# Kernel tuning notes

Measured on AMD Instinct MI355X. Metric: run time of the kernel, lower is better.

The kernel has to match this reference:

```python
import jax, jax.numpy as jnp
import numpy as np

B, N, D, H = 2, 2048, 1024, 16
DH = D // H  # head dim = 64


def setup_inputs() -> dict:
    key = jax.random.key(0)
    k1, k2, k3 = jax.random.split(key, 3)
    x = jax.random.normal(k1, (B, N, D), dtype=jnp.float32)
    # per-head Linear(D, 3*DH): stacked weights (H, D, 3*DH), biases (H, 3*DH)
    W_qkv = jax.random.normal(k2, (H, D, 3 * DH), dtype=jnp.float32) * 0.02
    b_qkv = jnp.zeros((H, 3 * DH), dtype=jnp.float32)
    W_proj = jax.random.normal(k3, (D, D), dtype=jnp.float32) * 0.02
    b_proj = jnp.zeros((D,), dtype=jnp.float32)
    return {"x": x, "W_qkv": W_qkv, "b_qkv": b_qkv, "W_proj": W_proj, "b_proj": b_proj}


def reference(x, W_qkv, b_qkv, W_proj, b_proj):
    b, n, d = x.shape
    h = W_qkv.shape[0]
    dh = W_qkv.shape[2] // 3
    # all heads' kqv projections at once: (B, H, N, 3*DH)
    qkv = jnp.einsum('bnd,hde->bhne', x, W_qkv) + b_qkv[None, :, None, :]
    # original chunks in order k, q, v
    k, q, v = jnp.split(qkv, 3, axis=-1)  # each (B, H, N, DH)
    # scores[b,h,n,m] = q_n . k_m / sqrt(dh)
    scores = jnp.einsum('bhnd,bhmd->bhnm', q, k) / jnp.sqrt(jnp.asarray(dh, x.dtype))
    causal = jnp.tril(jnp.ones((n, n), dtype=bool))
    scores = jnp.where(causal[None, None, :, :], scores, -jnp.inf)
    A = jax.nn.softmax(scores, axis=-1)
    out = jnp.einsum('bhnm,bhmd->bhnd', A, v)
    # concat heads (head-major order matches the torch cat over head list)
    out = out.transpose(0, 2, 1, 3).reshape(b, n, h * dh)
    return out @ W_proj + b_proj
```

## Files before the change

### kernel.cpp

```cpp
#include <hip/hip_runtime.h>
#include <hip/hip_bf16.h>

typedef __hip_bfloat16 HBF;
typedef __bf16 bf16x8 __attribute__((ext_vector_type(8)));
typedef __bf16 bf16x4 __attribute__((ext_vector_type(4)));
typedef float f32x4 __attribute__((ext_vector_type(4)));
typedef float float4v __attribute__((ext_vector_type(4)));

__device__ __forceinline__ float toF(float x) { return x; }
__device__ __forceinline__ float toF(HBF x) { return __bfloat162float(x); }

#define MFMA16(a, b, c) __builtin_amdgcn_mfma_f32_16x16x32_bf16((a), (b), (c), 0, 0, 0)
#define EXP2F(x) __builtin_amdgcn_exp2f(x)
#define QSCALE 0.18033688011112042f
#define MEMFENCE asm volatile("" ::: "memory")

__device__ __forceinline__ void gload_lds16(const HBF* g, HBF* l) {
  __builtin_amdgcn_global_load_lds((const __attribute__((address_space(1))) void*)g,
                                   (__attribute__((address_space(3))) void*)l, 16, 0, 0);
}

__global__ void prep_k(const float* __restrict__ x, HBF* __restrict__ xb,
                       const float* __restrict__ Wqkv, HBF* __restrict__ wqkv_t,
                       const float* __restrict__ Wproj, HBF* __restrict__ wproj_t) {
  const int bid = blockIdx.x, tid = threadIdx.x;
  if (bid < 4096) {
    int i = bid * 256 + tid;
    float4v a = reinterpret_cast<const float4v*>(x)[i];
    HBF o[4] = {__float2bfloat16(a.x), __float2bfloat16(a.y),
                __float2bfloat16(a.z), __float2bfloat16(a.w)};
    *reinterpret_cast<ulonglong1*>(&xb[i * 4]) = *reinterpret_cast<ulonglong1*>(o);
    return;
  }
  __shared__ float tile[32][33];
  const float* in;
  HBF* out;
  int R, C, gx, gy;
  size_t base;
  if (bid < 7168) {
    int t = bid - 4096;
    int gz = t / 192, rem = t % 192;
    gy = rem / 6; gx = rem % 6;
    R = 1024; C = 192;
    base = (size_t)gz * R * C;
    in = Wqkv; out = wqkv_t;
  } else {
    int t = bid - 7168;
    gy = t / 32; gx = t % 32;
    R = 1024; C = 1024;
    base = 0;
    in = Wproj; out = wproj_t;
  }
  int r0 = gy * 32, c0 = gx * 32;
  int tx = tid & 31, ty = tid >> 5;
#pragma unroll
  for (int i = ty; i < 32; i += 8)
    tile[i][tx] = in[base + (size_t)(r0 + i) * C + c0 + tx];
  __syncthreads();
#pragma unroll
  for (int i = ty; i < 32; i += 8)
    out[base + (size_t)(c0 + i) * R + r0 + tx] = __float2bfloat16(tile[tx][i]);
}

__launch_bounds__(512, 4)
__global__ void gemm_qkv_8ph(const HBF* __restrict__ A, const HBF* __restrict__ Bt,
                             const float* __restrict__ bias,
                             HBF* __restrict__ Kout, HBF* __restrict__ Qout,
                             HBF* __restrict__ Vtout) {
  __shared__ __align__(16) HBF As[2][8192];
  __shared__ __align__(16) HBF Bs[2][12288];
  const int tid = threadIdx.x, lane = tid & 63, w = tid >> 6;
  const int lo = lane & 15, g4 = lane >> 4;
  const int wr = w >> 2, wc = w & 3;
  const int s = ((int)blockIdx.x & 7) * 64 + ((int)blockIdx.x >> 3);
  const int bx = s & 15, by = s >> 4;
  const int m0 = by * 128, n0 = bx * 192;
  const int NT = 16;

  f32x4 acc[4][3];
#pragma unroll
  for (int i = 0; i < 4; i++)
#pragma unroll
    for (int j = 0; j < 3; j++) acc[i][j] = (f32x4){0.f, 0.f, 0.f, 0.f};
  bf16x8 af[4][2], bfr[3][2];

  const int rl0 = w * 8 + (lane >> 3);
  const int rl1 = 64 + rl0;
  const int kc0 = (lane & 7) ^ (rl0 & 7);
  const int kc1 = (lane & 7) ^ (rl1 & 7);

  auto stageA = [&](int kt) {
    HBF* base = &As[kt & 1][0];
    gload_lds16(A + (size_t)(m0 + rl0) * 1024 + kt * 64 + kc0 * 8, base + w * 512);
    gload_lds16(A + (size_t)(m0 + rl1) * 1024 + kt * 64 + kc1 * 8, base + 4096 + w * 512);
  };
  auto stageB = [&](int kt, int g) {
    gload_lds16(Bt + (size_t)(n0 + g * 64 + rl0) * 1024 + kt * 64 + kc0 * 8,
                &Bs[kt & 1][g * 4096] + w * 512);
  };
  auto ldA = [&](int bb, int mt, int ks) -> bf16x8 {
    int row = wr * 64 + mt * 16 + lo;
    return *reinterpret_cast<const bf16x8*>(&As[bb][row * 64 + ((ks * 32 + g4 * 8) ^ ((row & 7) * 8))]);
  };
  auto ldB = [&](int bb, int nt, int ks) -> bf16x8 {
    int row = wc * 48 + nt * 16 + lo;
    return *reinterpret_cast<const bf16x8*>(&Bs[bb][row * 64 + ((ks * 32 + g4 * 8) ^ ((row & 7) * 8))]);
  };

  stageA(0); stageB(0, 0); stageB(0, 1); stageB(0, 2);
  stageA(1);
  asm volatile("s_waitcnt vmcnt(2)" ::: "memory");
  __builtin_amdgcn_s_barrier();
  MEMFENCE;

  for (int t = 0; t < NT; ++t) {
    const int bb = t & 1;
#pragma unroll
    for (int mt = 0; mt < 4; ++mt) { af[mt][0] = ldA(bb, mt, 0); af[mt][1] = ldA(bb, mt, 1); }
#pragma unroll
    for (int nt = 0; nt < 2; ++nt) { bfr[nt][0] = ldB(bb, nt, 0); bfr[nt][1] = ldB(bb, nt, 1); }
    if (t + 1 < NT) stageB(t + 1, 0);
    MEMFENCE; __builtin_amdgcn_s_barrier(); MEMFENCE;
    __builtin_amdgcn_s_setprio(1);
#pragma unroll
    for (int mt = 0; mt < 4; ++mt)
#pragma unroll
      for (int nt = 0; nt < 2; ++nt)
#pragma unroll
        for (int ks = 0; ks < 2; ++ks) acc[mt][nt] = MFMA16(af[mt][ks], bfr[nt][ks], acc[mt][nt]);
    __builtin_amdgcn_s_setprio(0);
    MEMFENCE; __builtin_amdgcn_s_barrier(); MEMFENCE;
    bfr[2][0] = ldB(bb, 2, 0); bfr[2][1] = ldB(bb, 2, 1);
    if (t + 1 < NT) { stageB(t + 1, 1); stageB(t + 1, 2); }
    if (t + 2 < NT) stageA(t + 2);
    MEMFENCE; __builtin_amdgcn_s_barrier(); MEMFENCE;
    __builtin_amdgcn_s_setprio(1);
#pragma unroll
    for (int mt = 0; mt < 4; ++mt)
#pragma unroll
      for (int ks = 0; ks < 2; ++ks) acc[mt][2] = MFMA16(af[mt][ks], bfr[2][ks], acc[mt][2]);
    __builtin_amdgcn_s_setprio(0);
    if (t + 2 < NT) {
      asm volatile("s_waitcnt vmcnt(2)" ::: "memory");
    } else {
      asm volatile("s_waitcnt vmcnt(0)" ::: "memory");
    }
    __builtin_amdgcn_s_barrier();
    MEMFENCE;
  }

#pragma unroll
  for (int mt = 0; mt < 4; ++mt) {
    int mrow = m0 + wr * 64 + mt * 16 + g4 * 4;
#pragma unroll
    for (int nt = 0; nt < 3; ++nt) {
      int e = wc * 48 + nt * 16 + lo;
      float bv = bias[bx * 192 + e];
#pragma unroll
      for (int r = 0; r < 4; ++r) {
        int mm = mrow + r;
        int b = mm >> 11, n = mm & 2047;
        float v = acc[mt][nt][r] + bv;
        size_t bh64 = (size_t)(b * 16 + bx);
        if (e < 64)       Kout[(bh64 * 2048 + n) * 64 + e] = __float2bfloat16(v);
        else if (e < 128) Qout[(bh64 * 2048 + n) * 64 + e - 64] = __float2bfloat16(v * QSCALE);
        else              Vtout[(bh64 * 64 + (e - 128)) * 2048 + n] = __float2bfloat16(v);
      }
    }
  }
}

__launch_bounds__(256, 3)
__global__ void gemm_proj_k(const HBF* __restrict__ A, const HBF* __restrict__ Bt,
                            const float* __restrict__ bias, float* __restrict__ Cout) {
  __shared__ __align__(16) HBF As[2][4096];
  __shared__ __align__(16) HBF Bs[2][8192];
  const int tid = threadIdx.x, lane = tid & 63, w = tid >> 6;
  const int lo = lane & 15, g4 = lane >> 4;
  const int wrp = w >> 1, wcp = w & 1;
  const int s = ((int)blockIdx.x & 7) * 64 + ((int)blockIdx.x >> 3);
  const int bxn = s & 7, by = s >> 3;
  const int m0 = by * 64, n0 = bxn * 128;
  const int NT = 16;

  f32x4 acc[2][4];
#pragma unroll
  for (int i = 0; i < 2; i++)
#pragma unroll
    for (int j = 0; j < 4; j++) acc[i][j] = (f32x4){0.f, 0.f, 0.f, 0.f};
  bf16x8 af[2][2], bfr[4][2];

  const int rr = tid >> 3;
  const int ch = tid & 7;

  auto stageA = [&](int kt, int h) {
    int row = h * 32 + rr;
    gload_lds16(A + (size_t)(m0 + row) * 1024 + kt * 64 + ((ch ^ (row & 7)) * 8),
                &As[kt & 1][h * 2048] + w * 512);
  };
  auto stageB = [&](int kt, int g) {
    int row = g * 32 + rr;
    gload_lds16(Bt + (size_t)(n0 + row) * 1024 + kt * 64 + ((ch ^ (row & 7)) * 8),
                &Bs[kt & 1][g * 2048] + w * 512);
  };
  auto ldA = [&](int bb, int mt, int ks) -> bf16x8 {
    int row = wrp * 32 + mt * 16 + lo;
    return *reinterpret_cast<const bf16x8*>(&As[bb][row * 64 + ((ks * 32 + g4 * 8) ^ ((row & 7) * 8))]);
  };
  auto ldB = [&](int bb, int nt, int ks) -> bf16x8 {
    int row = wcp * 64 + nt * 16 + lo;
    return *reinterpret_cast<const bf16x8*>(&Bs[bb][row * 64 + ((ks * 32 + g4 * 8) ^ ((row & 7) * 8))]);
  };

  stageA(0, 0); stageA(0, 1);
  stageB(0, 0); stageB(0, 1); stageB(0, 2); stageB(0, 3);
  stageA(1, 0); stageA(1, 1);
  asm volatile("s_waitcnt vmcnt(2)" ::: "memory");
  __builtin_amdgcn_s_barrier();
  MEMFENCE;

  for (int t = 0; t < NT; ++t) {
    const int bb = t & 1;
#pragma unroll
    for (int mt = 0; mt < 2; ++mt) { af[mt][0] = ldA(bb, mt, 0); af[mt][1] = ldA(bb, mt, 1); }
#pragma unroll
    for (int nt = 0; nt < 2; ++nt) { bfr[nt][0] = ldB(bb, nt, 0); bfr[nt][1] = ldB(bb, nt, 1); }
    if (t + 1 < NT) { stageB(t + 1, 0); stageB(t + 1, 1); }
    MEMFENCE; __builtin_amdgcn_s_barrier(); MEMFENCE;
    __builtin_amdgcn_s_setprio(1);
#pragma unroll
    for (int mt = 0; mt < 2; ++mt)
#pragma unroll
      for (int nt = 0; nt < 2; ++nt)
#pragma unroll
        for (int ks = 0; ks < 2; ++ks) acc[mt][nt] = MFMA16(af[mt][ks], bfr[nt][ks], acc[mt][nt]);
    __builtin_amdgcn_s_setprio(0);
    MEMFENCE; __builtin_amdgcn_s_barrier(); MEMFENCE;
#pragma unroll
    for (int nt = 2; nt < 4; ++nt) { bfr[nt][0] = ldB(bb, nt, 0); bfr[nt][1] = ldB(bb, nt, 1); }
    if (t + 1 < NT) { stageB(t + 1, 2); stageB(t + 1, 3); }
    if (t + 2 < NT) { stageA(t + 2, 0); stageA(t + 2, 1); }
    MEMFENCE; __builtin_amdgcn_s_barrier(); MEMFENCE;
    __builtin_amdgcn_s_setprio(1);
#pragma unroll
    for (int mt = 0; mt < 2; ++mt)
#pragma unroll
      for (int nt = 2; nt < 4; ++nt)
#pragma unroll
        for (int ks = 0; ks < 2; ++ks) acc[mt][nt] = MFMA16(af[mt][ks], bfr[nt][ks], acc[mt][nt]);
    __builtin_amdgcn_s_setprio(0);
    if (t + 2 < NT) {
      asm volatile("s_waitcnt vmcnt(2)" ::: "memory");
    } else {
      asm volatile("s_waitcnt vmcnt(0)" ::: "memory");
    }
    __builtin_amdgcn_s_barrier();
    MEMFENCE;
  }

#pragma unroll
  for (int mt = 0; mt < 2; ++mt) {
    int mrow = m0 + wrp * 32 + mt * 16 + g4 * 4;
#pragma unroll
    for (int nt = 0; nt < 4; ++nt) {
      int col = n0 + wcp * 64 + nt * 16 + lo;
      float bv = bias[col];
#pragma unroll
      for (int r = 0; r < 4; ++r)
        Cout[(size_t)(mrow + r) * 1024 + col] = acc[mt][nt][r] + bv;
    }
  }
}

__launch_bounds__(256, 4)
__global__ void attn_fwd_k(const HBF* __restrict__ Qb, const HBF* __restrict__ Kb,
                           const HBF* __restrict__ Vt, HBF* __restrict__ Ob) {
  __shared__ __align__(16) HBF Ks[2][4096];
  __shared__ __align__(16) HBF Vs[2][4096];
  __shared__ __align__(16) HBF pLds[4][2048];
  const int tid = threadIdx.x;
  const int lane = tid & 63;
  const int w = tid >> 6;
  const int lo = lane & 15, g4 = lane >> 4;

  const int lin = blockIdx.x;
  const int xcd = lin & 7, c = lin >> 3;
  const int bh = xcd * 4 + (c & 3);
  const int j = 31 - (c >> 2);
  const int b = bh >> 4, h = bh & 15;
  const int qrow0 = j * 64 + w * 16;
  const int nkv = (j + 2) >> 1;

  const HBF* Qp = Qb + (size_t)bh * 2048 * 64;
  const HBF* Kp = Kb + (size_t)bh * 2048 * 64;
  const HBF* Vp = Vt + (size_t)bh * 64 * 2048;

  bf16x8 qf[2];
#pragma unroll
  for (int ds = 0; ds < 2; ds++)
    qf[ds] = *reinterpret_cast<const bf16x8*>(Qp + (size_t)(qrow0 + lo) * 64 + ds * 32 + g4 * 8);

  const f32x4 zero = {0.f, 0.f, 0.f, 0.f};
  f32x4 o[4];
  float m = -1e30f, l = 0.f;
#pragma unroll
  for (int j4 = 0; j4 < 4; j4++) o[j4] = zero;

  const int srow = (lane >> 3) & 7;
  const int sch = lane & 7;
  const int psw = (lo & 7) << 4;

  auto stage = [&](int kv0) {
#pragma unroll
    for (int sub = 0; sub < 2; sub++)
#pragma unroll
      for (int cc = 0; cc < 2; cc++) {
        int seg = w * 2 + cc;
        int row = seg * 8 + srow;
        gload_lds16(Kp + (size_t)(kv0 + sub * 64 + row) * 64 + ((sch ^ (row & 7)) * 8),
                    &Ks[sub][seg * 512]);
        gload_lds16(Vp + (size_t)row * 2048 + kv0 + sub * 64 + ((sch ^ (row & 7)) * 8),
                    &Vs[sub][seg * 512]);
      }
  };

  for (int t = 0; t < nkv; ++t) {
    const int kv0 = t * 128;
    stage(kv0);
    __syncthreads();

    f32x4 st[2][4];
#pragma unroll
    for (int sub = 0; sub < 2; sub++)
#pragma unroll
      for (int kt = 0; kt < 4; kt++) {
        int krow = kt * 16 + lo;
        bf16x8 kf0 = *reinterpret_cast<const bf16x8*>(&Ks[sub][krow * 64 + ((g4 ^ (krow & 7)) * 8)]);
        bf16x8 kf1 = *reinterpret_cast<const bf16x8*>(&Ks[sub][krow * 64 + (((4 + g4) ^ (krow & 7)) * 8)]);
        f32x4 z = zero;
        z = MFMA16(kf0, qf[0], z);
        z = MFMA16(kf1, qf[1], z);
        st[sub][kt] = z;
      }

    const int q = qrow0 + lo;
    float pmax = -1e30f;
    if (t == nkv - 1) {
#pragma unroll
      for (int sub = 0; sub < 2; sub++)
#pragma unroll
        for (int kt = 0; kt < 4; kt++)
#pragma unroll
          for (int r = 0; r < 4; r++) {
            int key = kv0 + sub * 64 + kt * 16 + g4 * 4 + r;
            float v = (key <= q) ? st[sub][kt][r] : -1e30f;
            st[sub][kt][r] = v;
            pmax = fmaxf(pmax, v);
          }
    } else {
#pragma unroll
      for (int sub = 0; sub < 2; sub++)
#pragma unroll
        for (int kt = 0; kt < 4; kt++)
#pragma unroll
          for (int r = 0; r < 4; r++) pmax = fmaxf(pmax, st[sub][kt][r]);
    }
    pmax = fmaxf(pmax, __shfl_xor(pmax, 16));
    pmax = fmaxf(pmax, __shfl_xor(pmax, 32));
    if (__any(pmax > m + 11.5f)) {
      float mn = fmaxf(m, pmax);
      float al = EXP2F(m - mn);
      m = mn;
      l *= al;
      float alr[4];
#pragma unroll
      for (int r = 0; r < 4; r++) alr[r] = __shfl(al, g4 * 4 + r);
#pragma unroll
      for (int j4 = 0; j4 < 4; j4++)
#pragma unroll
        for (int r = 0; r < 4; r++) o[j4][r] *= alr[r];
    }
#pragma unroll
    for (int sub = 0; sub < 2; sub++)
#pragma unroll
      for (int kt = 0; kt < 4; kt++)
#pragma unroll
        for (int r = 0; r < 4; r++) {
          float p = EXP2F(st[sub][kt][r] - m);
          st[sub][kt][r] = p;
          l += p;
        }
#pragma unroll
    for (int sub = 0; sub < 2; sub++)
#pragma unroll
      for (int kt = 0; kt < 4; kt++) {
        bf16x4 pk;
#pragma unroll
        for (int r = 0; r < 4; r++) pk[r] = (__bf16)st[sub][kt][r];
        *reinterpret_cast<bf16x4*>(
            &pLds[w][lo * 128 + (((sub * 128 + kt * 32 + g4 * 8) ^ psw) >> 1)]) = pk;
      }
    asm volatile("s_waitcnt lgkmcnt(0)" ::: "memory");
    __builtin_amdgcn_sched_barrier(0);

    bf16x8 pa[4];
#pragma unroll
    for (int ks = 0; ks < 4; ks++)
      pa[ks] = *reinterpret_cast<const bf16x8*>(
          &pLds[w][lo * 128 + (((ks * 64 + g4 * 16) ^ psw) >> 1)]);
#pragma unroll
    for (int j4 = 0; j4 < 4; j4++) {
      int vrow = j4 * 16 + lo;
#pragma unroll
      for (int ks = 0; ks < 4; ks++) {
        bf16x8 vb = *reinterpret_cast<const bf16x8*>(
            &Vs[ks >> 1][vrow * 64 + ((((ks & 1) * 4 + g4) ^ (vrow & 7)) * 8)]);
        o[j4] = MFMA16(pa[ks], vb, o[j4]);
      }
    }
    __syncthreads();
  }

  l += __shfl_xor(l, 16);
  l += __shfl_xor(l, 32);
  float linv = 1.f / l;
  float lr[4];
#pragma unroll
  for (int r = 0; r < 4; r++) lr[r] = __shfl(linv, g4 * 4 + r);
#pragma unroll
  for (int j4 = 0; j4 < 4; j4++)
#pragma unroll
    for (int r = 0; r < 4; r++) {
      int q = qrow0 + g4 * 4 + r;
      Ob[(size_t)(b * 2048 + q) * 1024 + h * 64 + j4 * 16 + lo] =
          __float2bfloat16(o[j4][r] * lr[r]);
    }
}

extern "C" void kernel_launch(void* const* d_in, const int* in_sizes, int n_in,
                              void* d_out, int out_size, void* d_ws, size_t ws_size,
                              hipStream_t stream) {
  const float* x      = (const float*)d_in[0];
  const float* W_qkv  = (const float*)d_in[1];
  const float* b_qkv  = (const float*)d_in[2];
  const float* W_proj = (const float*)d_in[3];
  const float* b_proj = (const float*)d_in[4];
  float* out = (float*)d_out;

  const int B = 2, N = 2048, D = 1024, H = 16, DH = 64;
  const int M = B * N;

  char* ws = (char*)d_ws;
  HBF* xb      = (HBF*)ws; ws += (size_t)M * D * 2;
  HBF* wqkv_t  = (HBF*)ws; ws += (size_t)H * 3 * DH * D * 2;
  HBF* wproj_t = (HBF*)ws; ws += (size_t)D * D * 2;
  HBF* Qb      = (HBF*)ws; ws += (size_t)B * H * N * DH * 2;
  HBF* Kb      = (HBF*)ws; ws += (size_t)B * H * N * DH * 2;
  HBF* Vt      = (HBF*)ws; ws += (size_t)B * H * DH * N * 2;
  HBF* Ob      = (HBF*)ws; ws += (size_t)M * D * 2;

  prep_k<<<8192, 256, 0, stream>>>(x, xb, W_qkv, wqkv_t, W_proj, wproj_t);
  gemm_qkv_8ph<<<512, 512, 0, stream>>>(xb, wqkv_t, b_qkv, Kb, Qb, Vt);
  attn_fwd_k<<<1024, 256, 0, stream>>>(Qb, Kb, Vt, Ob);
  gemm_proj_k<<<512, 256, 0, stream>>>(Ob, wproj_t, b_proj, out);
}
```

Before: 97.77 us.

## Double-buffer K/V tiles and give each warp two query tiles in attention

The attention kernel now handles 128 query rows per block, two 16-row tiles per warp, so each K/V tile loaded into LDS is reused across twice as many queries and the grid is halved. The K/V staging moves from a 128-key single buffer loaded synchronously to a 64-key double buffer that prefetches the next tile while the current one is computed. Per-warp causal activity flags skip MFMAs for query tiles that are fully masked. The cost is more registers (launch bounds drop from 4 to 3 blocks per SM), fewer blocks in flight, and a less even causal load per block.

```diff
diff --git a/kernel.cpp b/kernel.cpp
--- a/kernel.cpp
+++ b/kernel.cpp
@@ -272,12 +272,12 @@
   }
 }
 
-__launch_bounds__(256, 4)
+__launch_bounds__(256, 3)
 __global__ void attn_fwd_k(const HBF* __restrict__ Qb, const HBF* __restrict__ Kb,
                            const HBF* __restrict__ Vt, HBF* __restrict__ Ob) {
   __shared__ __align__(16) HBF Ks[2][4096];
   __shared__ __align__(16) HBF Vs[2][4096];
-  __shared__ __align__(16) HBF pLds[4][2048];
+  __shared__ __align__(16) HBF pLds[4][2][1024];
   const int tid = threadIdx.x;
   const int lane = tid & 63;
   const int w = tid >> 6;
@@ -286,155 +286,174 @@
   const int lin = blockIdx.x;
   const int xcd = lin & 7, c = lin >> 3;
   const int bh = xcd * 4 + (c & 3);
-  const int j = 31 - (c >> 2);
+  const int jb = 15 - (c >> 2);
   const int b = bh >> 4, h = bh & 15;
-  const int qrow0 = j * 64 + w * 16;
-  const int nkv = (j + 2) >> 1;
+  const int qw0 = jb * 128 + w * 32;
+  const int qw1 = qw0 + 16;
+  const int nkv = jb * 2 + 2;
 
   const HBF* Qp = Qb + (size_t)bh * 2048 * 64;
   const HBF* Kp = Kb + (size_t)bh * 2048 * 64;
   const HBF* Vp = Vt + (size_t)bh * 64 * 2048;
 
-  bf16x8 qf[2];
-#pragma unroll
-  for (int ds = 0; ds < 2; ds++)
-    qf[ds] = *reinterpret_cast<const bf16x8*>(Qp + (size_t)(qrow0 + lo) * 64 + ds * 32 + g4 * 8);
+  bf16x8 qf[2][2];
+#pragma unroll
+  for (int qt = 0; qt < 2; qt++)
+#pragma unroll
+    for (int ds = 0; ds < 2; ds++)
+      qf[qt][ds] = *reinterpret_cast<const bf16x8*>(
+          Qp + (size_t)(qw0 + qt * 16 + lo) * 64 + ds * 32 + g4 * 8);
 
   const f32x4 zero = {0.f, 0.f, 0.f, 0.f};
-  f32x4 o[4];
-  float m = -1e30f, l = 0.f;
-#pragma unroll
-  for (int j4 = 0; j4 < 4; j4++) o[j4] = zero;
+  f32x4 o[2][4];
+  float m[2] = {-1e30f, -1e30f}, l[2] = {0.f, 0.f};
+#pragma unroll
+  for (int qt = 0; qt < 2; qt++)
+#pragma unroll
+    for (int j4 = 0; j4 < 4; j4++) o[qt][j4] = zero;
 
   const int srow = (lane >> 3) & 7;
   const int sch = lane & 7;
   const int psw = (lo & 7) << 4;
 
-  auto stage = [&](int kv0) {
-#pragma unroll
-    for (int sub = 0; sub < 2; sub++)
-#pragma unroll
-      for (int cc = 0; cc < 2; cc++) {
-        int seg = w * 2 + cc;
-        int row = seg * 8 + srow;
-        gload_lds16(Kp + (size_t)(kv0 + sub * 64 + row) * 64 + ((sch ^ (row & 7)) * 8),
-                    &Ks[sub][seg * 512]);
-        gload_lds16(Vp + (size_t)row * 2048 + kv0 + sub * 64 + ((sch ^ (row & 7)) * 8),
-                    &Vs[sub][seg * 512]);
-      }
-  };
+  auto stage = [&](int kv0, int sb) {
+#pragma unroll
+    for (int cc = 0; cc < 2; cc++) {
+      int seg = w * 2 + cc;
+      int row = seg * 8 + srow;
+      gload_lds16(Kp + (size_t)(kv0 + row) * 64 + ((sch ^ (row & 7)) * 8), &Ks[sb][seg * 512]);
+      gload_lds16(Vp + (size_t)row * 2048 + kv0 + ((sch ^ (row & 7)) * 8), &Vs[sb][seg * 512]);
+    }
+  };
+
+  stage(0, 0);
+  __syncthreads();
 
   for (int t = 0; t < nkv; ++t) {
-    const int kv0 = t * 128;
-    stage(kv0);
-    __syncthreads();
+    const int kv0 = t * 64;
+    const int sb = t & 1;
+    if (t + 1 < nkv) stage(kv0 + 64, sb ^ 1);
+    const bool act0 = kv0 <= qw0 + 15;
+    const bool act1 = kv0 <= qw1 + 15;
 
     f32x4 st[2][4];
 #pragma unroll
-    for (int sub = 0; sub < 2; sub++)
-#pragma unroll
-      for (int kt = 0; kt < 4; kt++) {
-        int krow = kt * 16 + lo;
-        bf16x8 kf0 = *reinterpret_cast<const bf16x8*>(&Ks[sub][krow * 64 + ((g4 ^ (krow & 7)) * 8)]);
-        bf16x8 kf1 = *reinterpret_cast<const bf16x8*>(&Ks[sub][krow * 64 + (((4 + g4) ^ (krow & 7)) * 8)]);
+    for (int kt = 0; kt < 4; kt++) {
+      int krow = kt * 16 + lo;
+      bf16x8 kf0 = *reinterpret_cast<const bf16x8*>(&Ks[sb][krow * 64 + ((g4 ^ (krow & 7)) * 8)]);
+      bf16x8 kf1 = *reinterpret_cast<const bf16x8*>(&Ks[sb][krow * 64 + (((4 + g4) ^ (krow & 7)) * 8)]);
+      if (act1) {
         f32x4 z = zero;
-        z = MFMA16(kf0, qf[0], z);
-        z = MFMA16(kf1, qf[1], z);
-        st[sub][kt] = z;
-      }
-
-    const int q = qrow0 + lo;
-    float pmax = -1e30f;
-    if (t == nkv - 1) {
-#pragma unroll
-      for (int sub = 0; sub < 2; sub++)
+        z = MFMA16(kf0, qf[1][0], z);
+        z = MFMA16(kf1, qf[1][1], z);
+        st[1][kt] = z;
+      }
+      if (act0) {
+        f32x4 y = zero;
+        y = MFMA16(kf0, qf[0][0], y);
+        y = MFMA16(kf1, qf[0][1], y);
+        st[0][kt] = y;
+      }
+    }
+
+#pragma unroll
+    for (int qt = 0; qt < 2; qt++) {
+      if (!(qt ? act1 : act0)) continue;
+      const int qw = qt ? qw1 : qw0;
+      const int q = qw + lo;
+      float pmax = -1e30f;
+      if (kv0 + 63 > qw) {
 #pragma unroll
         for (int kt = 0; kt < 4; kt++)
 #pragma unroll
           for (int r = 0; r < 4; r++) {
-            int key = kv0 + sub * 64 + kt * 16 + g4 * 4 + r;
-            float v = (key <= q) ? st[sub][kt][r] : -1e30f;
-            st[sub][kt][r] = v;
+            int key = kv0 + kt * 16 + g4 * 4 + r;
+            float v = (key <= q) ? st[qt][kt][r] : -1e30f;
+            st[qt][kt][r] = v;
             pmax = fmaxf(pmax, v);
           }
-    } else {
-#pragma unroll
-      for (int sub = 0; sub < 2; sub++)
+      } else {
 #pragma unroll
         for (int kt = 0; kt < 4; kt++)
 #pragma unroll
-          for (int r = 0; r < 4; r++) pmax = fmaxf(pmax, st[sub][kt][r]);
-    }
-    pmax = fmaxf(pmax, __shfl_xor(pmax, 16));
-    pmax = fmaxf(pmax, __shfl_xor(pmax, 32));
-    if (__any(pmax > m + 11.5f)) {
-      float mn = fmaxf(m, pmax);
-      float al = EXP2F(m - mn);
-      m = mn;
-      l *= al;
-      float alr[4];
-#pragma unroll
-      for (int r = 0; r < 4; r++) alr[r] = __shfl(al, g4 * 4 + r);
-#pragma unroll
-      for (int j4 = 0; j4 < 4; j4++)
-#pragma unroll
-        for (int r = 0; r < 4; r++) o[j4][r] *= alr[r];
-    }
-#pragma unroll
-    for (int sub = 0; sub < 2; sub++)
+          for (int r = 0; r < 4; r++) pmax = fmaxf(pmax, st[qt][kt][r]);
+      }
+      pmax = fmaxf(pmax, __shfl_xor(pmax, 16));
+      pmax = fmaxf(pmax, __shfl_xor(pmax, 32));
+      if (__any(pmax > m[qt] + 11.5f)) {
+        float mn = fmaxf(m[qt], pmax);
+        float al = EXP2F(m[qt] - mn);
+        m[qt] = mn;
+        l[qt] *= al;
+        float alr[4];
+#pragma unroll
+        for (int r = 0; r < 4; r++) alr[r] = __shfl(al, g4 * 4 + r);
+#pragma unroll
+        for (int j4 = 0; j4 < 4; j4++)
+#pragma unroll
+          for (int r = 0; r < 4; r++) o[qt][j4][r] *= alr[r];
+      }
 #pragma unroll
       for (int kt = 0; kt < 4; kt++)
 #pragma unroll
         for (int r = 0; r < 4; r++) {
-          float p = EXP2F(st[sub][kt][r] - m);
-          st[sub][kt][r] = p;
-          l += p;
+          float p = EXP2F(st[qt][kt][r] - m[qt]);
+          st[qt][kt][r] = p;
+          l[qt] += p;
         }
-#pragma unroll
-    for (int sub = 0; sub < 2; sub++)
 #pragma unroll
       for (int kt = 0; kt < 4; kt++) {
         bf16x4 pk;
 #pragma unroll
-        for (int r = 0; r < 4; r++) pk[r] = (__bf16)st[sub][kt][r];
+        for (int r = 0; r < 4; r++) pk[r] = (__bf16)st[qt][kt][r];
         *reinterpret_cast<bf16x4*>(
-            &pLds[w][lo * 128 + (((sub * 128 + kt * 32 + g4 * 8) ^ psw) >> 1)]) = pk;
-      }
+            &pLds[w][qt][lo * 64 + (((kt * 32 + g4 * 8) ^ psw) >> 1)]) = pk;
+      }
+    }
     asm volatile("s_waitcnt lgkmcnt(0)" ::: "memory");
     __builtin_amdgcn_sched_barrier(0);
 
-    bf16x8 pa[4];
-#pragma unroll
-    for (int ks = 0; ks < 4; ks++)
-      pa[ks] = *reinterpret_cast<const bf16x8*>(
-          &pLds[w][lo * 128 + (((ks * 64 + g4 * 16) ^ psw) >> 1)]);
+    bf16x8 pa0[2], pa1[2];
+#pragma unroll
+    for (int ks = 0; ks < 2; ks++) {
+      if (act1) pa1[ks] = *reinterpret_cast<const bf16x8*>(
+          &pLds[w][1][lo * 64 + (((ks * 64 + g4 * 16) ^ psw) >> 1)]);
+      if (act0) pa0[ks] = *reinterpret_cast<const bf16x8*>(
+          &pLds[w][0][lo * 64 + (((ks * 64 + g4 * 16) ^ psw) >> 1)]);
+    }
 #pragma unroll
     for (int j4 = 0; j4 < 4; j4++) {
       int vrow = j4 * 16 + lo;
 #pragma unroll
-      for (int ks = 0; ks < 4; ks++) {
+      for (int ks = 0; ks < 2; ks++) {
         bf16x8 vb = *reinterpret_cast<const bf16x8*>(
-            &Vs[ks >> 1][vrow * 64 + ((((ks & 1) * 4 + g4) ^ (vrow & 7)) * 8)]);
-        o[j4] = MFMA16(pa[ks], vb, o[j4]);
+            &Vs[sb][vrow * 64 + (((ks * 4 + g4) ^ (vrow & 7)) * 8)]);
+        if (act1) o[1][j4] = MFMA16(pa1[ks], vb, o[1][j4]);
+        if (act0) o[0][j4] = MFMA16(pa0[ks], vb, o[0][j4]);
       }
     }
     __syncthreads();
   }
 
-  l += __shfl_xor(l, 16);
-  l += __shfl_xor(l, 32);
-  float linv = 1.f / l;
-  float lr[4];
-#pragma unroll
-  for (int r = 0; r < 4; r++) lr[r] = __shfl(linv, g4 * 4 + r);
-#pragma unroll
-  for (int j4 = 0; j4 < 4; j4++)
-#pragma unroll
-    for (int r = 0; r < 4; r++) {
-      int q = qrow0 + g4 * 4 + r;
-      Ob[(size_t)(b * 2048 + q) * 1024 + h * 64 + j4 * 16 + lo] =
-          __float2bfloat16(o[j4][r] * lr[r]);
-    }
+#pragma unroll
+  for (int qt = 0; qt < 2; qt++) {
+    float lv = l[qt];
+    lv += __shfl_xor(lv, 16);
+    lv += __shfl_xor(lv, 32);
+    float linv = 1.f / lv;
+    float lr[4];
+#pragma unroll
+    for (int r = 0; r < 4; r++) lr[r] = __shfl(linv, g4 * 4 + r);
+    const int qw = qt ? qw1 : qw0;
+#pragma unroll
+    for (int j4 = 0; j4 < 4; j4++)
+#pragma unroll
+      for (int r = 0; r < 4; r++) {
+        int q = qw + g4 * 4 + r;
+        Ob[(size_t)(b * 2048 + q) * 1024 + h * 64 + j4 * 16 + lo] =
+            __float2bfloat16(o[qt][j4][r] * lr[r]);
+      }
+  }
 }
 
 extern "C" void kernel_launch(void* const* d_in, const int* in_sizes, int n_in,
@@ -461,6 +480,6 @@
 
   prep_k<<<8192, 256, 0, stream>>>(x, xb, W_qkv, wqkv_t, W_proj, wproj_t);
   gemm_qkv_8ph<<<512, 512, 0, stream>>>(xb, wqkv_t, b_qkv, Kb, Qb, Vt);
-  attn_fwd_k<<<1024, 256, 0, stream>>>(Qb, Kb, Vt, Ob);
+  attn_fwd_k<<<512, 256, 0, stream>>>(Qb, Kb, Vt, Ob);
   gemm_proj_k<<<512, 256, 0, stream>>>(Ob, wproj_t, b_proj, out);
 }
```

Result: slower. 125.7 us (+28.6%).
